# Performance work log

Hardware: AMD Instinct MI355X
Metric: run time of the kernel (lower is better)

The kernel has to match this reference:

```python
import jax, jax.numpy as jnp
import numpy as np

NEIGHBOR_NUM = 10   # FLAGS.gcn_n_num
SUPPORT_NUM = 7     # FLAGS.gcn_sup_num


def _norm(x, axis=-1):
    # F.normalize: divide by norm clamped to 1e-12
    return x / jnp.clip(jnp.linalg.norm(x, axis=axis, keepdims=True), 1e-12)


def _knn(v, k):
    # pairwise squared-distance KNN, excluding self -> (b, n, k)
    d2 = jnp.sum(v * v, -1)
    dist = d2[:, :, None] + d2[:, None, :] - 2.0 * jnp.einsum('bic,bjc->bij', v, v)
    idx = jax.lax.top_k(-dist, k + 1)[1]
    return idx[:, :, 1:]


_gather = jax.vmap(lambda f, i: f[i])  # f:(v,c), i:(v,k) -> (v,k,c)


def _orl(feat, w):
    # hybrid-scope fusion: concat per-point feature with global mean, 1x1 conv, residual
    g = jnp.broadcast_to(feat.mean(1, keepdims=True), feat.shape)
    return jnp.einsum('bvc,oc->bvo', jnp.concatenate([feat, g], -1), w) + feat


def _surface(verts, n, dirs, ste_w, orl_w):
    # HSlayer_surface: directional supports on normalized neighbor offsets
    b, v, _ = verts.shape
    f_ste = jnp.einsum('bvc,oc->bvo', verts, ste_w)              # (b,v,K)
    dnorm = _norm(_gather(verts, _knn(verts, n)) - verts[:, :, None, :])  # (b,v,n,3)
    theta = jax.nn.relu(jnp.einsum('bvnc,cs->bvns', dnorm, _norm(dirs, 0)))  # (b,v,n,S*K)
    theta = theta.reshape(b, v, n, SUPPORT_NUM, -1)
    return _orl(theta.max(2).sum(2) + f_ste, orl_w)


def _hs(verts, fmap, n, w, bias, dirs, ste_w, orl_w, out_c):
    # HS_layer: support-weighted aggregation of projected neighbor features
    b, v, _ = verts.shape
    f_ste = jnp.einsum('bvc,oc->bvo', fmap, ste_w)
    idx = _knn(verts, n)
    dnorm = _norm(_gather(verts, idx) - verts[:, :, None, :])
    theta = jax.nn.relu(jnp.einsum('bvnc,cs->bvns', dnorm, _norm(dirs, 0)))  # (b,v,n,S*O)
    fout = fmap @ w + bias                        # (b,v,(S+1)*O)
    f_center = fout[..., :out_c]
    f_support = _gather(fout[..., out_c:], idx)   # (b,v,n,S*O)
    act = (theta * f_support).reshape(b, v, n, SUPPORT_NUM, out_c)
    return _orl(f_center + act.max(2).sum(2) + f_ste, orl_w)


def _bn(x, g, b, eps=1e-5):
    # BatchNorm1d (training mode, biased variance) over (batch, vertices)
    m = x.mean((0, 1))
    var = ((x - m) ** 2).mean((0, 1))
    return (x - m) * jax.lax.rsqrt(var + eps) * g + b


def _pool(verts, fmap, rate=4, k=4):
    # neighborhood max-pool then deterministic 1/rate subsample
    pooled = _gather(fmap, _knn(verts, k)).max(2)
    pn = verts.shape[1] // rate
    return verts[:, :pn], pooled[:, :pn]


def setup_inputs() -> dict:
    key = jax.random.key(0)
    ks = iter(jax.random.split(key, 40))
    r = lambda *s: jax.random.normal(next(ks), s, jnp.float32) * 0.05
    S = SUPPORT_NUM
    return dict(
        vertices=jax.random.normal(next(ks), (4, 4096, 3), jnp.float32),
        dirs0=r(3, S * 128), ste0=r(128, 3), orl0=r(128, 256),
        w1=r(128, (S + 1) * 128), b1=r((S + 1) * 128), dirs1=r(3, S * 128),
        ste1=r(128, 128), orl1=r(128, 256),
        bn1_g=jnp.ones(128, jnp.float32), bn1_b=jnp.zeros(128, jnp.float32),
        w2=r(128, (S + 1) * 256), b2=r((S + 1) * 256), dirs2=r(3, S * 256),
        ste2=r(256, 128), orl2=r(256, 512),
        bn2_g=jnp.ones(256, jnp.float32), bn2_b=jnp.zeros(256, jnp.float32),
        w3=r(256, (S + 1) * 256), b3=r((S + 1) * 256), dirs3=r(3, S * 256),
        ste3=r(256, 256), orl3=r(256, 512),
        bn3_g=jnp.ones(256, jnp.float32), bn3_b=jnp.zeros(256, jnp.float32),
        w4=r(256, (S + 1) * 512), b4=r((S + 1) * 512), dirs4=r(3, S * 512),
        ste4=r(512, 256), orl4=r(512, 1024),
    )


def reference(vertices, dirs0, ste0, orl0,
              w1, b1, dirs1, ste1, orl1, bn1_g, bn1_b,
              w2, b2, dirs2, ste2, orl2, bn2_g, bn2_b,
              w3, b3, dirs3, ste3, orl3, bn3_g, bn3_b,
              w4, b4, dirs4, ste4, orl4):
    n = NEIGHBOR_NUM
    fm0 = jax.nn.relu(_surface(vertices, n, dirs0, ste0, orl0))
    fm1 = jax.nn.relu(_bn(_hs(vertices, fm0, n, w1, b1, dirs1, ste1, orl1, 128), bn1_g, bn1_b))
    v1, fp1 = _pool(vertices, fm1)
    n1 = min(n, v1.shape[1] // 8)
    fm2 = jax.nn.relu(_bn(_hs(v1, fp1, n1, w2, b2, dirs2, ste2, orl2, 256), bn2_g, bn2_b))
    fm3 = jax.nn.relu(_bn(_hs(v1, fm2, n1, w3, b3, dirs3, ste3, orl3, 256), bn3_g, bn3_b))
    v2, fp2 = _pool(v1, fm3)
    n2 = min(n, v2.shape[1] // 8)
    fm4 = _hs(v2, fp2, n2, w4, b4, dirs4, ste4, orl4, 512)
    return fm4.max(1)  # (bs, 512)
```

## Files before the change

kernel.cpp:

```cpp
#include <hip/hip_runtime.h>

#define S_NUM 7
#define NB 10
#define NEG_INF (-3.402823466e38f)


__global__ void normalize_dirs_kernel(const float* __restrict__ dirs, float* __restrict__ out, int M) {
  int m = blockIdx.x * blockDim.x + threadIdx.x;
  if (m >= M) return;
  float a = dirs[m], b = dirs[M + m], c = dirs[2 * M + m];
  float L = fmaxf(sqrtf(a * a + b * b + c * c), 1e-12f);
  out[m] = a / L; out[M + m] = b / L; out[2 * M + m] = c / L;
}

__global__ void transpose_sub_kernel(const float* __restrict__ in, float* __restrict__ out,
                                     int R, int Cfull, int Csub) {
  int t = blockIdx.x * blockDim.x + threadIdx.x;
  if (t >= R * Csub) return;
  int r = t % R, c = t / R;
  out[(size_t)c * R + r] = in[(size_t)r * Cfull + c];
}

__global__ __launch_bounds__(256) void knn_kernel(const float* __restrict__ verts, int V, int bstride,
                                                  int* __restrict__ idx_out) {
  int wave = threadIdx.x >> 6;
  int lane = threadIdx.x & 63;
  int i = blockIdx.x * 4 + wave;
  int b = blockIdx.y;
  if (i >= V) return;
  const float* vb = verts + (size_t)b * bstride;
  float xi = vb[3 * i], yi = vb[3 * i + 1], zi = vb[3 * i + 2];
  float d2i = xi * xi + yi * yi + zi * zi;
  unsigned long long top[11];
#pragma unroll
  for (int t = 0; t < 11; ++t) top[t] = ~0ull;
  for (int j = lane; j < V; j += 64) {
    float xj = vb[3 * j], yj = vb[3 * j + 1], zj = vb[3 * j + 2];
    float d2j = xj * xj + yj * yj + zj * zj;
    float dt = xi * xj + yi * yj + zi * zj;
    float dist = (d2i + d2j) - 2.0f * dt;
    if (j == i) dist = -1.0f;
    unsigned int fb = __float_as_uint(dist);
    fb ^= ((unsigned int)((int)fb >> 31)) | 0x80000000u;
    unsigned long long key = ((unsigned long long)fb << 32) | (unsigned int)j;
    if (key < top[10]) {
      top[10] = key;
#pragma unroll
      for (int t = 10; t > 0; --t) {
        if (top[t] < top[t - 1]) { unsigned long long tm = top[t]; top[t] = top[t - 1]; top[t - 1] = tm; }
      }
    }
  }
#pragma unroll 1
  for (int t = 0; t < 11; ++t) {
    unsigned long long m = top[0];
#pragma unroll
    for (int o = 32; o > 0; o >>= 1) {
      unsigned long long other = __shfl_xor(m, o, 64);
      m = (other < m) ? other : m;
    }
    if (top[0] == m) {
#pragma unroll
      for (int q = 0; q < 10; ++q) top[q] = top[q + 1];
      top[10] = ~0ull;
    }
    if (t >= 1 && lane == 0)
      idx_out[((size_t)b * V + i) * NB + (t - 1)] = (int)(m & 0xffffffffu);
  }
}

__global__ __launch_bounds__(256) void gemm_kernel(
    const float* __restrict__ A, const float* __restrict__ B,
    const float* __restrict__ bias, const float* __restrict__ gt,
    const float* __restrict__ resid, float* __restrict__ C,
    int M, int N, int K, int rpb, int relu) {
  __shared__ float As[32][68];
  __shared__ float Bs[32][64];
  int bm = blockIdx.x * 64;
  int bn = blockIdx.y * 64;
  int tid = threadIdx.x;
  int tx = tid & 15, ty = tid >> 4;
  float acc[4][4] = {};
  for (int k0 = 0; k0 < K; k0 += 32) {
#pragma unroll
    for (int l = 0; l < 2; ++l) {
      int f = tid + l * 256;
      int row = f >> 3, kq = f & 7;
      float4 a = *reinterpret_cast<const float4*>(&A[(size_t)(bm + row) * K + k0 + kq * 4]);
      As[kq * 4 + 0][row] = a.x; As[kq * 4 + 1][row] = a.y;
      As[kq * 4 + 2][row] = a.z; As[kq * 4 + 3][row] = a.w;
    }
#pragma unroll
    for (int l = 0; l < 2; ++l) {
      int f = tid + l * 256;
      int row = f >> 4, cq = f & 15;
      float4 v = *reinterpret_cast<const float4*>(&B[(size_t)(k0 + row) * N + bn + cq * 4]);
      *reinterpret_cast<float4*>(&Bs[row][cq * 4]) = v;
    }
    __syncthreads();
#pragma unroll
    for (int kk = 0; kk < 32; ++kk) {
      float4 av = *reinterpret_cast<const float4*>(&As[kk][ty * 4]);
      float4 bv = *reinterpret_cast<const float4*>(&Bs[kk][tx * 4]);
      float am[4] = {av.x, av.y, av.z, av.w};
      float bb[4] = {bv.x, bv.y, bv.z, bv.w};
#pragma unroll
      for (int i2 = 0; i2 < 4; ++i2)
#pragma unroll
        for (int j2 = 0; j2 < 4; ++j2)
          acc[i2][j2] = fmaf(am[i2], bb[j2], acc[i2][j2]);
    }
    __syncthreads();
  }
#pragma unroll
  for (int i2 = 0; i2 < 4; ++i2) {
    int row = bm + ty * 4 + i2;
    int col0 = bn + tx * 4;
    float4 v;
    float* vv = reinterpret_cast<float*>(&v);
#pragma unroll
    for (int j2 = 0; j2 < 4; ++j2) {
      float t = acc[i2][j2];
      int col = col0 + j2;
      if (bias)  t += bias[col];
      if (resid) t += resid[(size_t)row * N + col];
      if (gt)    t += gt[(row / rpb) * N + col];
      if (relu)  t = fmaxf(t, 0.0f);
      vv[j2] = t;
    }
    *reinterpret_cast<float4*>(&C[(size_t)row * N + col0]) = v;
  }
}

__global__ __launch_bounds__(128) void surface0_kernel(const float* __restrict__ verts,
    const int* __restrict__ idx, const float* __restrict__ ndirs,
    const float* __restrict__ ste0, float* __restrict__ feat) {
  __shared__ float dn[NB][3];
  int b = blockIdx.y, v = blockIdx.x;
  const float* vb = verts + (size_t)b * 4096 * 3;
  int tid = threadIdx.x;
  if (tid < NB) {
    int j = idx[((size_t)b * 4096 + v) * NB + tid];
    float dx = vb[3 * j] - vb[3 * v];
    float dy = vb[3 * j + 1] - vb[3 * v + 1];
    float dz = vb[3 * j + 2] - vb[3 * v + 2];
    float L = fmaxf(sqrtf(dx * dx + dy * dy + dz * dz), 1e-12f);
    dn[tid][0] = dx / L; dn[tid][1] = dy / L; dn[tid][2] = dz / L;
  }
  __syncthreads();
  int c = tid;
  float acc = vb[3 * v] * ste0[c * 3] + vb[3 * v + 1] * ste0[c * 3 + 1] + vb[3 * v + 2] * ste0[c * 3 + 2];
#pragma unroll
  for (int s = 0; s < S_NUM; ++s) {
    float w0 = ndirs[s * 128 + c], w1 = ndirs[896 + s * 128 + c], w2 = ndirs[1792 + s * 128 + c];
    float mx = NEG_INF;
#pragma unroll
    for (int n = 0; n < NB; ++n) {
      float th = fmaxf(dn[n][0] * w0 + dn[n][1] * w1 + dn[n][2] * w2, 0.0f);
      mx = fmaxf(mx, th);
    }
    acc += mx;
  }
  feat[((size_t)b * 4096 + v) * 128 + c] = acc;
}

template <int C>
__global__ void hs_kernel(const float* __restrict__ verts, int V,
                          const int* __restrict__ idx, const float* __restrict__ ndirs,
                          const float* __restrict__ fout, const float* __restrict__ fste,
                          float* __restrict__ feat) {
  __shared__ float dn[NB][3];
  __shared__ int nbr[NB];
  int b = blockIdx.y, v = blockIdx.x;
  const float* vb = verts + (size_t)b * 4096 * 3;
  int tid = threadIdx.x;
  if (tid < NB) {
    int j = idx[((size_t)b * V + v) * NB + tid];
    nbr[tid] = j;
    float dx = vb[3 * j] - vb[3 * v];
    float dy = vb[3 * j + 1] - vb[3 * v + 1];
    float dz = vb[3 * j + 2] - vb[3 * v + 2];
    float L = fmaxf(sqrtf(dx * dx + dy * dy + dz * dz), 1e-12f);
    dn[tid][0] = dx / L; dn[tid][1] = dy / L; dn[tid][2] = dz / L;
  }
  __syncthreads();
  int c = tid;
  size_t row = (size_t)b * V + v;
  float w0[S_NUM], w1[S_NUM], w2[S_NUM];
#pragma unroll
  for (int s = 0; s < S_NUM; ++s) {
    w0[s] = ndirs[s * C + c];
    w1[s] = ndirs[S_NUM * C + s * C + c];
    w2[s] = ndirs[2 * S_NUM * C + s * C + c];
  }
  float mx[S_NUM];
#pragma unroll
  for (int s = 0; s < S_NUM; ++s) mx[s] = NEG_INF;
  for (int n = 0; n < NB; ++n) {
    float d0 = dn[n][0], d1 = dn[n][1], d2 = dn[n][2];
    const float* fb = fout + ((size_t)b * V + nbr[n]) * (8 * C) + C + c;
#pragma unroll
    for (int s = 0; s < S_NUM; ++s) {
      float th = fmaxf(d0 * w0[s] + d1 * w1[s] + d2 * w2[s], 0.0f);
      mx[s] = fmaxf(mx[s], th * fb[(size_t)s * C]);
    }
  }
  float acc = fout[row * (8 * C) + c] + fste[row * C + c];
#pragma unroll
  for (int s = 0; s < S_NUM; ++s) acc += mx[s];
  feat[row * C + c] = acc;
}


__global__ void colsum_kernel(const float* __restrict__ x, double* __restrict__ sums,
                              int V, int C, int chunk) {
  int b = blockIdx.x, c = threadIdx.x;
  int r0 = blockIdx.y * chunk;
  int r1 = min(r0 + chunk, V);
  float s = 0.f;
  for (int r = r0; r < r1; ++r) s += x[((size_t)b * V + r) * C + c];
  atomicAdd(&sums[b * C + c], (double)s);
}

__global__ void gterm_kernel(const double* __restrict__ sums, const float* __restrict__ orl,
                             float* __restrict__ gt, int C, int O, double invV) {
  int b = blockIdx.x;
  int o = blockIdx.y * 64 + threadIdx.x;
  if (o >= O) return;
  float acc = 0.f;
  for (int c = 0; c < C; ++c)
    acc += (float)(sums[b * C + c] * invV) * orl[(size_t)o * (2 * C) + C + c];
  gt[b * O + o] = acc;
}

__global__ void bnstat_kernel(const float* __restrict__ x, double* __restrict__ stats,
                              int rows, int C, int chunk) {
  int c = threadIdx.x;
  int r0 = blockIdx.x * chunk;
  int r1 = min(r0 + chunk, rows);
  float s1 = 0.f, s2 = 0.f;
  for (int r = r0; r < r1; ++r) {
    float v = x[(size_t)r * C + c];
    s1 += v; s2 += v * v;
  }
  atomicAdd(&stats[c], (double)s1);
  atomicAdd(&stats[C + c], (double)s2);
}

__global__ void bnapply_kernel(const float* __restrict__ x, const double* __restrict__ stats,
                               const float* __restrict__ g, const float* __restrict__ bta,
                               float* __restrict__ y, int total, int C, double invN) {
  int i = blockIdx.x * blockDim.x + threadIdx.x;
  if (i >= total) return;
  int c = i % C;
  double m = stats[c] * invN;
  double var = stats[C + c] * invN - m * m;
  double inv = 1.0 / sqrt(var + 1e-5);
  float r = (float)(((double)x[i] - m) * inv) * g[c] + bta[c];
  y[i] = fmaxf(r, 0.0f);
}

template <int C>
__global__ void pool_kernel(const float* __restrict__ fm, const int* __restrict__ idx,
                            float* __restrict__ fp, int Vin) {
  int b = blockIdx.y, p = blockIdx.x, c = threadIdx.x;
  const int* ip = idx + ((size_t)b * Vin + p) * NB;
  float m = NEG_INF;
#pragma unroll
  for (int j = 0; j < 4; ++j)
    m = fmaxf(m, fm[((size_t)b * Vin + ip[j]) * C + c]);
  fp[((size_t)b * gridDim.x + p) * C + c] = m;
}

__global__ void finalmax_kernel(const float* __restrict__ fm4, float* __restrict__ out) {
  int b = blockIdx.x;
  int o = blockIdx.y * 256 + threadIdx.x;
  float m = NEG_INF;
  for (int v = 0; v < 256; ++v)
    m = fmaxf(m, fm4[((size_t)b * 256 + v) * 512 + o]);
  out[b * 512 + o] = m;
}


extern "C" void kernel_launch(void* const* d_in, const int* in_sizes, int n_in,
                              void* d_out, int out_size, void* d_ws, size_t ws_size,
                              hipStream_t stream) {
  const float* verts = (const float*)d_in[0];
  const float* dirs0 = (const float*)d_in[1];
  const float* ste0  = (const float*)d_in[2];
  const float* orl0  = (const float*)d_in[3];
  const float* w1    = (const float*)d_in[4];
  const float* b1    = (const float*)d_in[5];
  const float* dirs1 = (const float*)d_in[6];
  const float* ste1  = (const float*)d_in[7];
  const float* orl1  = (const float*)d_in[8];
  const float* bn1g  = (const float*)d_in[9];
  const float* bn1b  = (const float*)d_in[10];
  const float* w2    = (const float*)d_in[11];
  const float* b2    = (const float*)d_in[12];
  const float* dirs2 = (const float*)d_in[13];
  const float* ste2  = (const float*)d_in[14];
  const float* orl2  = (const float*)d_in[15];
  const float* bn2g  = (const float*)d_in[16];
  const float* bn2b  = (const float*)d_in[17];
  const float* w3    = (const float*)d_in[18];
  const float* b3    = (const float*)d_in[19];
  const float* dirs3 = (const float*)d_in[20];
  const float* ste3  = (const float*)d_in[21];
  const float* orl3  = (const float*)d_in[22];
  const float* bn3g  = (const float*)d_in[23];
  const float* bn3b  = (const float*)d_in[24];
  const float* w4    = (const float*)d_in[25];
  const float* b4    = (const float*)d_in[26];
  const float* dirs4 = (const float*)d_in[27];
  const float* ste4  = (const float*)d_in[28];
  const float* orl4  = (const float*)d_in[29];

  char* base = (char*)d_ws;
  size_t off = 0;
  auto alloc = [&](size_t bytes) -> void* {
    off = (off + 255) & ~(size_t)255;
    void* p = base + off;
    off += bytes;
    return p;
  };

  float* nd0  = (float*)alloc(3 * 896 * 4);
  float* nd1  = (float*)alloc(3 * 896 * 4);
  float* nd2  = (float*)alloc(3 * 1792 * 4);
  float* nd3  = (float*)alloc(3 * 1792 * 4);
  float* nd4  = (float*)alloc(3 * 3584 * 4);
  float* sT1  = (float*)alloc(128 * 128 * 4);
  float* sT2  = (float*)alloc(128 * 256 * 4);
  float* sT3  = (float*)alloc(256 * 256 * 4);
  float* sT4  = (float*)alloc(256 * 512 * 4);
  float* oA0  = (float*)alloc(128 * 128 * 4);
  float* oA1  = (float*)alloc(128 * 128 * 4);
  float* oA2  = (float*)alloc(256 * 256 * 4);
  float* oA3  = (float*)alloc(256 * 256 * 4);
  float* oA4  = (float*)alloc(512 * 512 * 4);
  int*   idx0 = (int*)alloc((size_t)4 * 4096 * NB * 4);
  int*   idx1 = (int*)alloc((size_t)4 * 1024 * NB * 4);
  int*   idx2 = (int*)alloc((size_t)4 * 256 * NB * 4);
  double* gsum  = (double*)alloc(4 * 512 * 8);
  float*  gterm = (float*)alloc(4 * 512 * 4);
  double* stats = (double*)alloc(2 * 256 * 8);
  float* Rfout = (float*)alloc((size_t)16384 * 1024 * 4);
  float* Rfeat = (float*)alloc((size_t)16384 * 128 * 4);
  float* Rtmp  = (float*)alloc((size_t)16384 * 128 * 4);
  float* Rfste = (float*)alloc((size_t)16384 * 128 * 4);
  float* Rfm   = (float*)alloc((size_t)16384 * 128 * 4);
  float* Rfp   = (float*)alloc((size_t)4 * 1024 * 128 * 4);
  (void)in_sizes; (void)n_in; (void)out_size; (void)ws_size;

  auto gemm = [&](const float* A, const float* B, const float* bias, const float* gt,
                  const float* resid, float* C, int M, int N, int K, int rpb, int relu) {
    gemm_kernel<<<dim3(M / 64, N / 64), 256, 0, stream>>>(A, B, bias, gt, resid, C, M, N, K, rpb ? rpb : 1, relu);
  };

  normalize_dirs_kernel<<<(896 + 255) / 256, 256, 0, stream>>>(dirs0, nd0, 896);
  normalize_dirs_kernel<<<(896 + 255) / 256, 256, 0, stream>>>(dirs1, nd1, 896);
  normalize_dirs_kernel<<<(1792 + 255) / 256, 256, 0, stream>>>(dirs2, nd2, 1792);
  normalize_dirs_kernel<<<(1792 + 255) / 256, 256, 0, stream>>>(dirs3, nd3, 1792);
  normalize_dirs_kernel<<<(3584 + 255) / 256, 256, 0, stream>>>(dirs4, nd4, 3584);
  transpose_sub_kernel<<<(128 * 128 + 255) / 256, 256, 0, stream>>>(ste1, sT1, 128, 128, 128);
  transpose_sub_kernel<<<(256 * 128 + 255) / 256, 256, 0, stream>>>(ste2, sT2, 256, 128, 128);
  transpose_sub_kernel<<<(256 * 256 + 255) / 256, 256, 0, stream>>>(ste3, sT3, 256, 256, 256);
  transpose_sub_kernel<<<(512 * 256 + 255) / 256, 256, 0, stream>>>(ste4, sT4, 512, 256, 256);
  transpose_sub_kernel<<<(128 * 128 + 255) / 256, 256, 0, stream>>>(orl0, oA0, 128, 256, 128);
  transpose_sub_kernel<<<(128 * 128 + 255) / 256, 256, 0, stream>>>(orl1, oA1, 128, 256, 128);
  transpose_sub_kernel<<<(256 * 256 + 255) / 256, 256, 0, stream>>>(orl2, oA2, 256, 512, 256);
  transpose_sub_kernel<<<(256 * 256 + 255) / 256, 256, 0, stream>>>(orl3, oA3, 256, 512, 256);
  transpose_sub_kernel<<<(512 * 512 + 255) / 256, 256, 0, stream>>>(orl4, oA4, 512, 1024, 512);

  const int VSTRIDE = 4096 * 3;

  knn_kernel<<<dim3(4096 / 4, 4), 256, 0, stream>>>(verts, 4096, VSTRIDE, idx0);

  surface0_kernel<<<dim3(4096, 4), 128, 0, stream>>>(verts, idx0, nd0, ste0, Rfeat);
  hipMemsetAsync(gsum, 0, 4 * 512 * 8, stream);
  colsum_kernel<<<dim3(4, 32), 128, 0, stream>>>(Rfeat, gsum, 4096, 128, 128);
  gterm_kernel<<<dim3(4, 2), 64, 0, stream>>>(gsum, orl0, gterm, 128, 128, 1.0 / 4096);
  gemm(Rfeat, oA0, nullptr, gterm, Rfeat, Rtmp, 16384, 128, 128, 4096, 1);

  gemm(Rtmp, w1, b1, nullptr, nullptr, Rfout, 16384, 1024, 128, 0, 0);
  gemm(Rtmp, sT1, nullptr, nullptr, nullptr, Rfste, 16384, 128, 128, 0, 0);
  hs_kernel<128><<<dim3(4096, 4), 128, 0, stream>>>(verts, 4096, idx0, nd1, Rfout, Rfste, Rfeat);
  hipMemsetAsync(gsum, 0, 4 * 512 * 8, stream);
  colsum_kernel<<<dim3(4, 32), 128, 0, stream>>>(Rfeat, gsum, 4096, 128, 128);
  gterm_kernel<<<dim3(4, 2), 64, 0, stream>>>(gsum, orl1, gterm, 128, 128, 1.0 / 4096);
  gemm(Rfeat, oA1, nullptr, gterm, Rfeat, Rtmp, 16384, 128, 128, 4096, 0);
  hipMemsetAsync(stats, 0, 2 * 256 * 8, stream);
  bnstat_kernel<<<128, 128, 0, stream>>>(Rtmp, stats, 16384, 128, 128);
  bnapply_kernel<<<(16384 * 128 + 255) / 256, 256, 0, stream>>>(Rtmp, stats, bn1g, bn1b, Rfm, 16384 * 128, 128, 1.0 / 16384);
  pool_kernel<128><<<dim3(1024, 4), 128, 0, stream>>>(Rfm, idx0, Rfp, 4096);
  knn_kernel<<<dim3(1024 / 4, 4), 256, 0, stream>>>(verts, 1024, VSTRIDE, idx1);

  gemm(Rfp, w2, b2, nullptr, nullptr, Rfout, 4096, 2048, 128, 0, 0);
  gemm(Rfp, sT2, nullptr, nullptr, nullptr, Rfste, 4096, 256, 128, 0, 0);
  hs_kernel<256><<<dim3(1024, 4), 256, 0, stream>>>(verts, 1024, idx1, nd2, Rfout, Rfste, Rfeat);
  hipMemsetAsync(gsum, 0, 4 * 512 * 8, stream);
  colsum_kernel<<<dim3(4, 8), 256, 0, stream>>>(Rfeat, gsum, 1024, 256, 128);
  gterm_kernel<<<dim3(4, 4), 64, 0, stream>>>(gsum, orl2, gterm, 256, 256, 1.0 / 1024);
  gemm(Rfeat, oA2, nullptr, gterm, Rfeat, Rtmp, 4096, 256, 256, 1024, 0);
  hipMemsetAsync(stats, 0, 2 * 256 * 8, stream);
  bnstat_kernel<<<32, 256, 0, stream>>>(Rtmp, stats, 4096, 256, 128);
  bnapply_kernel<<<(4096 * 256 + 255) / 256, 256, 0, stream>>>(Rtmp, stats, bn2g, bn2b, Rfm, 4096 * 256, 256, 1.0 / 4096);

  gemm(Rfm, w3, b3, nullptr, nullptr, Rfout, 4096, 2048, 256, 0, 0);
  gemm(Rfm, sT3, nullptr, nullptr, nullptr, Rfste, 4096, 256, 256, 0, 0);
  hs_kernel<256><<<dim3(1024, 4), 256, 0, stream>>>(verts, 1024, idx1, nd3, Rfout, Rfste, Rfeat);
  hipMemsetAsync(gsum, 0, 4 * 512 * 8, stream);
  colsum_kernel<<<dim3(4, 8), 256, 0, stream>>>(Rfeat, gsum, 1024, 256, 128);
  gterm_kernel<<<dim3(4, 4), 64, 0, stream>>>(gsum, orl3, gterm, 256, 256, 1.0 / 1024);
  gemm(Rfeat, oA3, nullptr, gterm, Rfeat, Rtmp, 4096, 256, 256, 1024, 0);
  hipMemsetAsync(stats, 0, 2 * 256 * 8, stream);
  bnstat_kernel<<<32, 256, 0, stream>>>(Rtmp, stats, 4096, 256, 128);
  bnapply_kernel<<<(4096 * 256 + 255) / 256, 256, 0, stream>>>(Rtmp, stats, bn3g, bn3b, Rfm, 4096 * 256, 256, 1.0 / 4096);
  pool_kernel<256><<<dim3(256, 4), 256, 0, stream>>>(Rfm, idx1, Rfp, 1024);
  knn_kernel<<<dim3(256 / 4, 4), 256, 0, stream>>>(verts, 256, VSTRIDE, idx2);

  gemm(Rfp, w4, b4, nullptr, nullptr, Rfout, 1024, 4096, 256, 0, 0);
  gemm(Rfp, sT4, nullptr, nullptr, nullptr, Rfste, 1024, 512, 256, 0, 0);
  hs_kernel<512><<<dim3(256, 4), 512, 0, stream>>>(verts, 256, idx2, nd4, Rfout, Rfste, Rfeat);
  hipMemsetAsync(gsum, 0, 4 * 512 * 8, stream);
  colsum_kernel<<<dim3(4, 2), 512, 0, stream>>>(Rfeat, gsum, 256, 512, 128);
  gterm_kernel<<<dim3(4, 8), 64, 0, stream>>>(gsum, orl4, gterm, 512, 512, 1.0 / 256);
  gemm(Rfeat, oA4, nullptr, gterm, Rfeat, Rtmp, 1024, 512, 512, 256, 0);

  finalmax_kernel<<<dim3(4, 2), 256, 0, stream>>>(Rtmp, (float*)d_out);
}
```

Before: 1.285 ms.

## Batch setup kernels, pack points as float4, and template the KNN kernel

Merges the five direction-normalization launches and nine transpose launches into one launch each, switching segments on blockIdx.y. Adds a pass that packs vertices into float4 (x,y,z,|p|^2) so KNN does one vector load per candidate instead of recomputing the squared norm. The KNN kernel is templated on V: it fills the first 11 keys directly, sorts them with an odd-even network, then uses a branch-free insertion for the remaining candidates. The separate BN-stats memsets are folded into the gsum memset by zeroing a contiguous span, which relies on the allocation order keeping those buffers adjacent.

```diff
diff --git a/kernel.cpp b/kernel.cpp
--- a/kernel.cpp
+++ b/kernel.cpp
@@ -5,49 +5,104 @@
 #define NEG_INF (-3.402823466e38f)
 
 
-__global__ void normalize_dirs_kernel(const float* __restrict__ dirs, float* __restrict__ out, int M) {
+struct NormSeg { const float* src; float* dst; int M; };
+
+__global__ void normalize_all_kernel(NormSeg s0, NormSeg s1, NormSeg s2, NormSeg s3, NormSeg s4) {
+  NormSeg s;
+  switch (blockIdx.y) {
+    case 0: s = s0; break;
+    case 1: s = s1; break;
+    case 2: s = s2; break;
+    case 3: s = s3; break;
+    default: s = s4; break;
+  }
   int m = blockIdx.x * blockDim.x + threadIdx.x;
-  if (m >= M) return;
-  float a = dirs[m], b = dirs[M + m], c = dirs[2 * M + m];
+  if (m >= s.M) return;
+  float a = s.src[m], b = s.src[s.M + m], c = s.src[2 * s.M + m];
   float L = fmaxf(sqrtf(a * a + b * b + c * c), 1e-12f);
-  out[m] = a / L; out[M + m] = b / L; out[2 * M + m] = c / L;
-}
-
-__global__ void transpose_sub_kernel(const float* __restrict__ in, float* __restrict__ out,
-                                     int R, int Cfull, int Csub) {
+  s.dst[m] = a / L; s.dst[s.M + m] = b / L; s.dst[2 * s.M + m] = c / L;
+}
+
+struct TSeg { const float* in; float* out; int R, Cfull, Csub; };
+
+__global__ void transpose_all_kernel(TSeg t0, TSeg t1, TSeg t2, TSeg t3, TSeg t4,
+                                     TSeg t5, TSeg t6, TSeg t7, TSeg t8) {
+  TSeg s;
+  switch (blockIdx.y) {
+    case 0: s = t0; break; case 1: s = t1; break; case 2: s = t2; break;
+    case 3: s = t3; break; case 4: s = t4; break; case 5: s = t5; break;
+    case 6: s = t6; break; case 7: s = t7; break; default: s = t8; break;
+  }
   int t = blockIdx.x * blockDim.x + threadIdx.x;
-  if (t >= R * Csub) return;
-  int r = t % R, c = t / R;
-  out[(size_t)c * R + r] = in[(size_t)r * Cfull + c];
-}
-
-__global__ __launch_bounds__(256) void knn_kernel(const float* __restrict__ verts, int V, int bstride,
+  if (t >= s.R * s.Csub) return;
+  int r = t % s.R, c = t / s.R;
+  s.out[(size_t)c * s.R + r] = s.in[(size_t)r * s.Cfull + c];
+}
+
+__global__ void pack_points_kernel(const float* __restrict__ verts, float4* __restrict__ pts, int total) {
+  int t = blockIdx.x * blockDim.x + threadIdx.x;
+  if (t >= total) return;
+  float x = verts[3 * t], y = verts[3 * t + 1], z = verts[3 * t + 2];
+  float d2 = x * x + y * y + z * z;
+  pts[t] = make_float4(x, y, z, d2);
+}
+
+__device__ __forceinline__ unsigned long long knn_key(float dist, int j) {
+  unsigned int fb = __float_as_uint(dist);
+  fb ^= ((unsigned int)((int)fb >> 31)) | 0x80000000u;
+  return ((unsigned long long)fb << 32) | (unsigned int)j;
+}
+
+template <int V>
+__global__ __launch_bounds__(256) void knn_kernel(const float4* __restrict__ pts,
                                                   int* __restrict__ idx_out) {
+  constexpr int ITERS = V / 64;
+  constexpr int FILL = (ITERS < 11) ? ITERS : 11;
   int wave = threadIdx.x >> 6;
   int lane = threadIdx.x & 63;
   int i = blockIdx.x * 4 + wave;
   int b = blockIdx.y;
-  if (i >= V) return;
-  const float* vb = verts + (size_t)b * bstride;
-  float xi = vb[3 * i], yi = vb[3 * i + 1], zi = vb[3 * i + 2];
-  float d2i = xi * xi + yi * yi + zi * zi;
+  const float4* pb = pts + (size_t)b * 4096;
+  float4 pi = pb[i];
   unsigned long long top[11];
 #pragma unroll
   for (int t = 0; t < 11; ++t) top[t] = ~0ull;
-  for (int j = lane; j < V; j += 64) {
-    float xj = vb[3 * j], yj = vb[3 * j + 1], zj = vb[3 * j + 2];
-    float d2j = xj * xj + yj * yj + zj * zj;
-    float dt = xi * xj + yi * yj + zi * zj;
-    float dist = (d2i + d2j) - 2.0f * dt;
+  const float4* pl = pb + lane;
+#pragma unroll
+  for (int t = 0; t < FILL; ++t) {
+    int j = lane + t * 64;
+    float4 pj = pl[t * 64];
+    float dt = pi.x * pj.x + pi.y * pj.y + pi.z * pj.z;
+    float dist = (pi.w + pj.w) - 2.0f * dt;
     if (j == i) dist = -1.0f;
-    unsigned int fb = __float_as_uint(dist);
-    fb ^= ((unsigned int)((int)fb >> 31)) | 0x80000000u;
-    unsigned long long key = ((unsigned long long)fb << 32) | (unsigned int)j;
+    top[t] = knn_key(dist, j);
+  }
+#pragma unroll
+  for (int p = 0; p < 11; ++p) {
+#pragma unroll
+    for (int q = (p & 1); q + 1 < 11; q += 2) {
+      unsigned long long a = top[q], bb = top[q + 1];
+      bool cgt = a > bb;
+      top[q] = cgt ? bb : a;
+      top[q + 1] = cgt ? a : bb;
+    }
+  }
+#pragma unroll 2
+  for (int t = FILL; t < ITERS; ++t) {
+    int j = lane + t * 64;
+    float4 pj = pl[t * 64];
+    float dt = pi.x * pj.x + pi.y * pj.y + pi.z * pj.z;
+    float dist = (pi.w + pj.w) - 2.0f * dt;
+    if (j == i) dist = -1.0f;
+    unsigned long long key = knn_key(dist, j);
     if (key < top[10]) {
-      top[10] = key;
-#pragma unroll
-      for (int t = 10; t > 0; --t) {
-        if (top[t] < top[t - 1]) { unsigned long long tm = top[t]; top[t] = top[t - 1]; top[t - 1] = tm; }
+      unsigned long long ck = key;
+#pragma unroll
+      for (int q = 0; q < 11; ++q) {
+        unsigned long long a = top[q];
+        bool cl = ck < a;
+        top[q] = cl ? ck : a;
+        ck = cl ? a : ck;
       }
     }
   }
@@ -339,12 +394,14 @@
   float* oA2  = (float*)alloc(256 * 256 * 4);
   float* oA3  = (float*)alloc(256 * 256 * 4);
   float* oA4  = (float*)alloc(512 * 512 * 4);
+  float4* pts = (float4*)alloc((size_t)4 * 4096 * 16);
   int*   idx0 = (int*)alloc((size_t)4 * 4096 * NB * 4);
   int*   idx1 = (int*)alloc((size_t)4 * 1024 * NB * 4);
   int*   idx2 = (int*)alloc((size_t)4 * 256 * NB * 4);
   double* gsum  = (double*)alloc(4 * 512 * 8);
   float*  gterm = (float*)alloc(4 * 512 * 4);
   double* stats = (double*)alloc(2 * 256 * 8);
+  size_t zspan = (size_t)((char*)(stats + 2 * 256) - (char*)gsum);
   float* Rfout = (float*)alloc((size_t)16384 * 1024 * 4);
   float* Rfeat = (float*)alloc((size_t)16384 * 128 * 4);
   float* Rtmp  = (float*)alloc((size_t)16384 * 128 * 4);
@@ -358,27 +415,21 @@
     gemm_kernel<<<dim3(M / 64, N / 64), 256, 0, stream>>>(A, B, bias, gt, resid, C, M, N, K, rpb ? rpb : 1, relu);
   };
 
-  normalize_dirs_kernel<<<(896 + 255) / 256, 256, 0, stream>>>(dirs0, nd0, 896);
-  normalize_dirs_kernel<<<(896 + 255) / 256, 256, 0, stream>>>(dirs1, nd1, 896);
-  normalize_dirs_kernel<<<(1792 + 255) / 256, 256, 0, stream>>>(dirs2, nd2, 1792);
-  normalize_dirs_kernel<<<(1792 + 255) / 256, 256, 0, stream>>>(dirs3, nd3, 1792);
-  normalize_dirs_kernel<<<(3584 + 255) / 256, 256, 0, stream>>>(dirs4, nd4, 3584);
-  transpose_sub_kernel<<<(128 * 128 + 255) / 256, 256, 0, stream>>>(ste1, sT1, 128, 128, 128);
-  transpose_sub_kernel<<<(256 * 128 + 255) / 256, 256, 0, stream>>>(ste2, sT2, 256, 128, 128);
-  transpose_sub_kernel<<<(256 * 256 + 255) / 256, 256, 0, stream>>>(ste3, sT3, 256, 256, 256);
-  transpose_sub_kernel<<<(512 * 256 + 255) / 256, 256, 0, stream>>>(ste4, sT4, 512, 256, 256);
-  transpose_sub_kernel<<<(128 * 128 + 255) / 256, 256, 0, stream>>>(orl0, oA0, 128, 256, 128);
-  transpose_sub_kernel<<<(128 * 128 + 255) / 256, 256, 0, stream>>>(orl1, oA1, 128, 256, 128);
-  transpose_sub_kernel<<<(256 * 256 + 255) / 256, 256, 0, stream>>>(orl2, oA2, 256, 512, 256);
-  transpose_sub_kernel<<<(256 * 256 + 255) / 256, 256, 0, stream>>>(orl3, oA3, 256, 512, 256);
-  transpose_sub_kernel<<<(512 * 512 + 255) / 256, 256, 0, stream>>>(orl4, oA4, 512, 1024, 512);
-
-  const int VSTRIDE = 4096 * 3;
-
-  knn_kernel<<<dim3(4096 / 4, 4), 256, 0, stream>>>(verts, 4096, VSTRIDE, idx0);
+  normalize_all_kernel<<<dim3(14, 5), 256, 0, stream>>>(
+      NormSeg{dirs0, nd0, 896}, NormSeg{dirs1, nd1, 896}, NormSeg{dirs2, nd2, 1792},
+      NormSeg{dirs3, nd3, 1792}, NormSeg{dirs4, nd4, 3584});
+  transpose_all_kernel<<<dim3(1024, 9), 256, 0, stream>>>(
+      TSeg{ste1, sT1, 128, 128, 128}, TSeg{ste2, sT2, 256, 128, 128},
+      TSeg{ste3, sT3, 256, 256, 256}, TSeg{ste4, sT4, 512, 256, 256},
+      TSeg{orl0, oA0, 128, 256, 128}, TSeg{orl1, oA1, 128, 256, 128},
+      TSeg{orl2, oA2, 256, 512, 256}, TSeg{orl3, oA3, 256, 512, 256},
+      TSeg{orl4, oA4, 512, 1024, 512});
+  pack_points_kernel<<<(4 * 4096 + 255) / 256, 256, 0, stream>>>(verts, pts, 4 * 4096);
+
+  knn_kernel<4096><<<dim3(4096 / 4, 4), 256, 0, stream>>>(pts, idx0);
 
   surface0_kernel<<<dim3(4096, 4), 128, 0, stream>>>(verts, idx0, nd0, ste0, Rfeat);
-  hipMemsetAsync(gsum, 0, 4 * 512 * 8, stream);
+  hipMemsetAsync(gsum, 0, zspan, stream);
   colsum_kernel<<<dim3(4, 32), 128, 0, stream>>>(Rfeat, gsum, 4096, 128, 128);
   gterm_kernel<<<dim3(4, 2), 64, 0, stream>>>(gsum, orl0, gterm, 128, 128, 1.0 / 4096);
   gemm(Rfeat, oA0, nullptr, gterm, Rfeat, Rtmp, 16384, 128, 128, 4096, 1);
@@ -386,44 +437,41 @@
   gemm(Rtmp, w1, b1, nullptr, nullptr, Rfout, 16384, 1024, 128, 0, 0);
   gemm(Rtmp, sT1, nullptr, nullptr, nullptr, Rfste, 16384, 128, 128, 0, 0);
   hs_kernel<128><<<dim3(4096, 4), 128, 0, stream>>>(verts, 4096, idx0, nd1, Rfout, Rfste, Rfeat);
-  hipMemsetAsync(gsum, 0, 4 * 512 * 8, stream);
+  hipMemsetAsync(gsum, 0, zspan, stream);
   colsum_kernel<<<dim3(4, 32), 128, 0, stream>>>(Rfeat, gsum, 4096, 128, 128);
   gterm_kernel<<<dim3(4, 2), 64, 0, stream>>>(gsum, orl1, gterm, 128, 128, 1.0 / 4096);
   gemm(Rfeat, oA1, nullptr, gterm, Rfeat, Rtmp, 16384, 128, 128, 4096, 0);
-  hipMemsetAsync(stats, 0, 2 * 256 * 8, stream);
   bnstat_kernel<<<128, 128, 0, stream>>>(Rtmp, stats, 16384, 128, 128);
   bnapply_kernel<<<(16384 * 128 + 255) / 256, 256, 0, stream>>>(Rtmp, stats, bn1g, bn1b, Rfm, 16384 * 128, 128, 1.0 / 16384);
   pool_kernel<128><<<dim3(1024, 4), 128, 0, stream>>>(Rfm, idx0, Rfp, 4096);
-  knn_kernel<<<dim3(1024 / 4, 4), 256, 0, stream>>>(verts, 1024, VSTRIDE, idx1);
+  knn_kernel<1024><<<dim3(1024 / 4, 4), 256, 0, stream>>>(pts, idx1);
 
   gemm(Rfp, w2, b2, nullptr, nullptr, Rfout, 4096, 2048, 128, 0, 0);
   gemm(Rfp, sT2, nullptr, nullptr, nullptr, Rfste, 4096, 256, 128, 0, 0);
   hs_kernel<256><<<dim3(1024, 4), 256, 0, stream>>>(verts, 1024, idx1, nd2, Rfout, Rfste, Rfeat);
-  hipMemsetAsync(gsum, 0, 4 * 512 * 8, stream);
+  hipMemsetAsync(gsum, 0, zspan, stream);
   colsum_kernel<<<dim3(4, 8), 256, 0, stream>>>(Rfeat, gsum, 1024, 256, 128);
   gterm_kernel<<<dim3(4, 4), 64, 0, stream>>>(gsum, orl2, gterm, 256, 256, 1.0 / 1024);
   gemm(Rfeat, oA2, nullptr, gterm, Rfeat, Rtmp, 4096, 256, 256, 1024, 0);
-  hipMemsetAsync(stats, 0, 2 * 256 * 8, stream);
   bnstat_kernel<<<32, 256, 0, stream>>>(Rtmp, stats, 4096, 256, 128);
   bnapply_kernel<<<(4096 * 256 + 255) / 256, 256, 0, stream>>>(Rtmp, stats, bn2g, bn2b, Rfm, 4096 * 256, 256, 1.0 / 4096);
 
   gemm(Rfm, w3, b3, nullptr, nullptr, Rfout, 4096, 2048, 256, 0, 0);
   gemm(Rfm, sT3, nullptr, nullptr, nullptr, Rfste, 4096, 256, 256, 0, 0);
   hs_kernel<256><<<dim3(1024, 4), 256, 0, stream>>>(verts, 1024, idx1, nd3, Rfout, Rfste, Rfeat);
-  hipMemsetAsync(gsum, 0, 4 * 512 * 8, stream);
+  hipMemsetAsync(gsum, 0, zspan, stream);
   colsum_kernel<<<dim3(4, 8), 256, 0, stream>>>(Rfeat, gsum, 1024, 256, 128);
   gterm_kernel<<<dim3(4, 4), 64, 0, stream>>>(gsum, orl3, gterm, 256, 256, 1.0 / 1024);
   gemm(Rfeat, oA3, nullptr, gterm, Rfeat, Rtmp, 4096, 256, 256, 1024, 0);
-  hipMemsetAsync(stats, 0, 2 * 256 * 8, stream);
   bnstat_kernel<<<32, 256, 0, stream>>>(Rtmp, stats, 4096, 256, 128);
   bnapply_kernel<<<(4096 * 256 + 255) / 256, 256, 0, stream>>>(Rtmp, stats, bn3g, bn3b, Rfm, 4096 * 256, 256, 1.0 / 4096);
   pool_kernel<256><<<dim3(256, 4), 256, 0, stream>>>(Rfm, idx1, Rfp, 1024);
-  knn_kernel<<<dim3(256 / 4, 4), 256, 0, stream>>>(verts, 256, VSTRIDE, idx2);
+  knn_kernel<256><<<dim3(256 / 4, 4), 256, 0, stream>>>(pts, idx2);
 
   gemm(Rfp, w4, b4, nullptr, nullptr, Rfout, 1024, 4096, 256, 0, 0);
   gemm(Rfp, sT4, nullptr, nullptr, nullptr, Rfste, 1024, 512, 256, 0, 0);
   hs_kernel<512><<<dim3(256, 4), 512, 0, stream>>>(verts, 256, idx2, nd4, Rfout, Rfste, Rfeat);
-  hipMemsetAsync(gsum, 0, 4 * 512 * 8, stream);
+  hipMemsetAsync(gsum, 0, zspan, stream);
   colsum_kernel<<<dim3(4, 2), 512, 0, stream>>>(Rfeat, gsum, 256, 512, 128);
   gterm_kernel<<<dim3(4, 8), 64, 0, stream>>>(gsum, orl4, gterm, 512, 512, 1.0 / 256);
   gemm(Rfeat, oA4, nullptr, gterm, Rfeat, Rtmp, 1024, 512, 512, 256, 0);
```

Result: no change. 1.290 ms (+0.4%).
